# Kernel tuning notes

Measured on AMD Instinct MI355X. Metric: run time of the kernel, lower is better.

## Reference

```python
import jax, jax.numpy as jnp
import numpy as np

N = 50000
E = 800000
IN_C = 64
OUT_C = 64
K = 2
GATE_C = IN_C + OUT_C
LAMBDA_MAX = 2.0


def _lap_norm(edge_index, edge_weight, n):
    # PyG ChebConv norm: sym Laplacian L = I - D^-1/2 A D^-1/2, scaled 2L/lmax - I.
    # With lambda_max=2 the diagonal term is (2/lmax)*1 - 1 = 0, so only the
    # off-diagonal weights -(2/lmax) * w_norm remain.
    row, col = edge_index[0], edge_index[1]
    deg = jax.ops.segment_sum(edge_weight, row, num_segments=n)
    dinv = jnp.where(deg > 0, jax.lax.rsqrt(jnp.where(deg > 0, deg, 1.0)), 0.0)
    lw = -(2.0 / LAMBDA_MAX) * edge_weight * dinv[row] * dinv[col]
    diag = jnp.full((n,), 2.0 / LAMBDA_MAX - 1.0, edge_weight.dtype)  # zeros for lmax=2
    return row, col, lw, diag


def _cheb_conv(x, row, col, lw, diag, Ws, b):
    # Ws: [K, C_in, C_out]; Tx_0 = x, Tx_1 = L_hat x, Tx_k = 2 L_hat Tx_{k-1} - Tx_{k-2}
    n = x.shape[0]

    def prop(h):  # L_hat @ h  via edge gather/scatter + diagonal
        msg = lw[:, None] * h[col]                      # [E, C]
        return jax.ops.segment_sum(msg, row, num_segments=n) + diag[:, None] * h

    Tx0 = x
    out = Tx0 @ Ws[0]
    Tx1 = prop(x)
    out = out + Tx1 @ Ws[1]
    for k in range(2, K):
        Tx2 = 2.0 * prop(Tx1) - Tx0
        out = out + Tx2 @ Ws[k]
        Tx0, Tx1 = Tx1, Tx2
    return out + b


def setup_inputs() -> dict:
    key = jax.random.key(0)
    ks = jax.random.split(key, 10)
    scale = 1.0 / np.sqrt(GATE_C)
    x = jax.random.normal(ks[0], (N, IN_C), jnp.float32)
    edge_index = jax.random.randint(ks[1], (2, E), 0, N, jnp.int64)
    edge_weight = jax.random.uniform(ks[2], (E,), jnp.float32)
    hidden_state = jax.random.normal(ks[3], (N, OUT_C), jnp.float32)
    Wz = jax.random.normal(ks[4], (K, GATE_C, OUT_C), jnp.float32) * scale
    Wr = jax.random.normal(ks[5], (K, GATE_C, OUT_C), jnp.float32) * scale
    Wh = jax.random.normal(ks[6], (K, GATE_C, OUT_C), jnp.float32) * scale
    bz = jnp.zeros((OUT_C,), jnp.float32)
    br = jnp.zeros((OUT_C,), jnp.float32)
    bh = jnp.zeros((OUT_C,), jnp.float32)
    return {"x": x, "edge_index": edge_index, "edge_weight": edge_weight,
            "hidden_state": hidden_state, "Wz": Wz, "bz": bz,
            "Wr": Wr, "br": br, "Wh": Wh, "bh": bh}


def reference(x, edge_index, edge_weight, hidden_state, Wz, bz, Wr, br, Wh, bh):
    n = x.shape[0]
    row, col, lw, diag = _lap_norm(edge_index, edge_weight, n)
    gate_input = jnp.concatenate([x, hidden_state], axis=-1)          # [N, GATE_C]
    z = jax.nn.sigmoid(_cheb_conv(gate_input, row, col, lw, diag, Wz, bz))
    r = jax.nn.sigmoid(_cheb_conv(gate_input, row, col, lw, diag, Wr, br))
    cand_in = jnp.concatenate([x, r * hidden_state], axis=-1)
    h_tilde = jnp.tanh(_cheb_conv(cand_in, row, col, lw, diag, Wh, bh))
    return (1.0 - z) * hidden_state + z * h_tilde
```

## Files before the change

### kernel.cpp

```cpp
#include <hip/hip_runtime.h>
#include <cstdint>

#define N_NODES 50000
#define N_EDGES 800000
#define C 64
#define SLOTS 64
#define B_N 120
#define NB 417
#define PCAP 2560
#define STG_BLOCKS 126
#define STG_CHUNK 6350

typedef __attribute__((ext_vector_type(8))) short bf16x8;
typedef __attribute__((ext_vector_type(4))) float f32x4;

static constexpr size_t OFF_GCUR = 0;
static constexpr size_t OFF_DINV = 512;
static constexpr size_t OFF_CNT  = 50688;
static constexpr size_t OFF_BZR  = 100864;
static constexpr size_t OFF_BH   = 117248;
static constexpr size_t OFF_CSR  = 125440;
static constexpr size_t OFF_XH   = OFF_CSR + (size_t)N_NODES * 64;
static constexpr size_t OFF_XB   = OFF_XH + (size_t)N_NODES * C;
static constexpr size_t OFF_HB   = OFF_XB + (size_t)N_NODES * C / 2;
static constexpr size_t OFF_PXB  = OFF_HB + (size_t)N_NODES * C / 2;
static constexpr size_t OFF_PHB  = OFF_PXB + (size_t)N_NODES * C / 2;
static constexpr size_t OFF_RHB  = OFF_PHB + (size_t)N_NODES * C / 2;
static constexpr size_t OFF_RHD  = OFF_RHB + (size_t)N_NODES * C / 2;
static constexpr size_t OFF_STG  = OFF_PXB;

__device__ __forceinline__ short f2bf(float f) {
    unsigned u = __float_as_uint(f);
    u += 0x7fffu + ((u >> 16) & 1u);
    return (short)(u >> 16);
}
__device__ __forceinline__ float bf_lo(unsigned v) { return __uint_as_float(v << 16); }
__device__ __forceinline__ float bf_hi(unsigned v) { return __uint_as_float(v & 0xffff0000u); }
__device__ __forceinline__ float bfu(unsigned short v) { return __uint_as_float((unsigned)v << 16); }
__device__ __forceinline__ float fast_sigmoid(float v) { return 1.f / (1.f + __expf(-v)); }
__device__ __forceinline__ float fast_tanh(float v) { return 1.f - 2.f / (__expf(2.f * v) + 1.f); }

__global__ __launch_bounds__(256) void zero_pack_kernel(
        int* __restrict__ gcur,
        const float* __restrict__ Wz, const float* __restrict__ Wr,
        const float* __restrict__ Wh,
        short* __restrict__ Bzr, short* __restrict__ Bh) {
    if (blockIdx.x == 24) {
        gcur[threadIdx.x] = 0;
        gcur[256 + threadIdx.x] = 0;
        return;
    }
    int gid = blockIdx.x * 256 + threadIdx.x;
    if (gid < 4096) {
        int ktct = gid >> 6, lane = gid & 63;
        int kt = ktct >> 3, ct = ktct & 7;
        int colg = ct * 16 + (lane & 15);
        int k0 = kt * 32 + (lane >> 4) * 8;
        const float* W = (colg < 64) ? Wz : Wr;
        int c = colg & 63;
        short v[8];
        #pragma unroll
        for (int j = 0; j < 8; ++j) {
            int k = k0 + j;
            v[j] = f2bf(W[(k >> 7) * (128 * 64) + (k & 127) * 64 + c]);
        }
        *(bf16x8*)(Bzr + (size_t)ktct * 512 + lane * 8) = *(bf16x8*)v;
    } else {
        int idx = gid - 4096;
        int ktct = idx >> 6, lane = idx & 63;
        int kt = ktct >> 2, ct = ktct & 3;
        int colg = ct * 16 + (lane & 15);
        int k0 = kt * 32 + (lane >> 4) * 8;
        short v[8];
        #pragma unroll
        for (int j = 0; j < 8; ++j) {
            int k = k0 + j;
            v[j] = f2bf(Wh[(k >> 7) * (128 * 64) + (k & 127) * 64 + colg]);
        }
        *(bf16x8*)(Bh + (size_t)ktct * 512 + lane * 8) = *(bf16x8*)v;
    }
}

__global__ __launch_bounds__(512) void stage_kernel(
        const int* __restrict__ row, const int* __restrict__ col,
        const float* __restrict__ w,
        int* __restrict__ gcur, uint2* __restrict__ stg) {
    __shared__ int lcnt[NB];
    __shared__ int lbase[NB];
    int tid = threadIdx.x;
    int e0 = blockIdx.x * STG_CHUNK;
    int e1 = min(e0 + STG_CHUNK, N_EDGES);
    for (int i = tid; i < NB; i += 512) lcnt[i] = 0;
    __syncthreads();
    for (int e = e0 + tid; e < e1; e += 512)
        atomicAdd(&lcnt[row[e] / B_N], 1);
    __syncthreads();
    for (int i = tid; i < NB; i += 512) {
        int c = lcnt[i];
        lbase[i] = c ? atomicAdd(&gcur[i], c) : 0;
        lcnt[i] = 0;
    }
    __syncthreads();
    for (int e = e0 + tid; e < e1; e += 512) {
        int r = row[e];
        int b = r / B_N;
        int off = atomicAdd(&lcnt[b], 1);
        int pos = lbase[b] + off;
        unsigned cw = ((unsigned)col[e] << 16) | (unsigned short)f2bf(w[e]);
        if (pos < PCAP)
            stg[(size_t)b * PCAP + pos] = make_uint2((unsigned)(r - b * B_N), cw);
    }
}

__global__ __launch_bounds__(256) void sort_kernel(
        const int* __restrict__ gcur, const uint2* __restrict__ stg,
        const float* __restrict__ x, const float* __restrict__ h,
        unsigned* __restrict__ csr, int* __restrict__ cnt, float* __restrict__ dinv,
        unsigned* __restrict__ xh,
        unsigned short* __restrict__ xb, unsigned short* __restrict__ hb) {
    __shared__ int lcnt[B_N];
    __shared__ int lbase[B_N];
    __shared__ float ldeg[B_N];
    __shared__ float ldv[B_N];
    __shared__ int scanb[128];
    __shared__ unsigned lbuf[PCAP];
    __shared__ unsigned char lnode[PCAP];
    int b = blockIdx.x, tid = threadIdx.x;
    int n0 = b * B_N;
    int m = min(gcur[b], PCAP);
    for (int i = tid; i < B_N; i += 256) { lcnt[i] = 0; ldeg[i] = 0.f; }
    __syncthreads();
    const uint2* s = stg + (size_t)b * PCAP;
    for (int i = tid; i < m; i += 256) {
        uint2 e = s[i];
        atomicAdd(&lcnt[e.x], 1);
        atomicAdd(&ldeg[e.x], bf_lo(e.y));
    }
    __syncthreads();
    if (tid < 128) scanb[tid] = (tid < B_N) ? lcnt[tid] : 0;
    __syncthreads();
    for (int d = 1; d < 128; d <<= 1) {
        int v = 0;
        if (tid < 128 && tid >= d) v = scanb[tid - d];
        __syncthreads();
        if (tid < 128) scanb[tid] += v;
        __syncthreads();
    }
    if (tid < B_N) { lbase[tid] = scanb[tid] - lcnt[tid]; lcnt[tid] = 0; }
    __syncthreads();
    for (int i = tid; i < m; i += 256) {
        uint2 e = s[i];
        int off = atomicAdd(&lcnt[e.x], 1);
        int p = lbase[e.x] + off;
        lbuf[p] = e.y;
        lnode[p] = (unsigned char)e.x;
    }
    __syncthreads();
    for (int i = tid; i < m; i += 256) {
        int nl = lnode[i];
        int pos = i - lbase[nl];
        csr[(size_t)(n0 + nl) * SLOTS + pos] = lbuf[i];
    }
    if (tid < B_N) {
        int node = n0 + tid;
        if (node < N_NODES) {
            cnt[node] = lcnt[tid];
            float d = ldeg[tid];
            float dv = (d > 0.f) ? rsqrtf(d) : 0.f;
            dinv[node] = dv;
            ldv[tid] = dv;
        } else ldv[tid] = 0.f;
    }
    __syncthreads();
    for (int i = tid; i < B_N * 16; i += 256) {
        int g = n0 * 16 + i;
        if (g >= N_NODES * 16) continue;
        float dv = ldv[i >> 4];
        float4 xv = ((const float4*)x)[g];
        float4 hv = ((const float4*)h)[g];
        uint4 o;
        o.x = ((unsigned)(unsigned short)f2bf(hv.x * dv) << 16) | (unsigned short)f2bf(xv.x * dv);
        o.y = ((unsigned)(unsigned short)f2bf(hv.y * dv) << 16) | (unsigned short)f2bf(xv.y * dv);
        o.z = ((unsigned)(unsigned short)f2bf(hv.z * dv) << 16) | (unsigned short)f2bf(xv.z * dv);
        o.w = ((unsigned)(unsigned short)f2bf(hv.w * dv) << 16) | (unsigned short)f2bf(xv.w * dv);
        ((uint4*)xh)[g] = o;
        ((short4*)xb)[g] = make_short4(f2bf(xv.x), f2bf(xv.y), f2bf(xv.z), f2bf(xv.w));
        ((short4*)hb)[g] = make_short4(f2bf(hv.x), f2bf(hv.y), f2bf(hv.z), f2bf(hv.w));
    }
}

__global__ __launch_bounds__(256) void prop2_gather_kernel(
        const int* __restrict__ cnt, const unsigned* __restrict__ csr,
        const float* __restrict__ dinv, const unsigned* __restrict__ xh,
        unsigned short* __restrict__ Pxb, unsigned short* __restrict__ Phb) {
    int n = (blockIdx.x * 256 + threadIdx.x) >> 6;
    int lane = threadIdx.x & 63;
    if (n >= N_NODES) return;
    int m = min(cnt[n], SLOTS);
    const unsigned* s = csr + (size_t)n * SLOTS;
    float ax = 0.f, ah = 0.f;
    int e = 0;
    for (; e + 4 <= m; e += 4) {
        unsigned p0 = s[e], p1 = s[e + 1], p2 = s[e + 2], p3 = s[e + 3];
        unsigned v0 = xh[(p0 >> 16) * C + lane];
        unsigned v1 = xh[(p1 >> 16) * C + lane];
        unsigned v2 = xh[(p2 >> 16) * C + lane];
        unsigned v3 = xh[(p3 >> 16) * C + lane];
        float w0 = bf_lo(p0), w1 = bf_lo(p1), w2 = bf_lo(p2), w3 = bf_lo(p3);
        ax = fmaf(w0, bf_lo(v0), ax);  ah = fmaf(w0, bf_hi(v0), ah);
        ax = fmaf(w1, bf_lo(v1), ax);  ah = fmaf(w1, bf_hi(v1), ah);
        ax = fmaf(w2, bf_lo(v2), ax);  ah = fmaf(w2, bf_hi(v2), ah);
        ax = fmaf(w3, bf_lo(v3), ax);  ah = fmaf(w3, bf_hi(v3), ah);
    }
    for (; e < m; ++e) {
        unsigned p = s[e];
        unsigned v = xh[(p >> 16) * C + lane];
        float wv = bf_lo(p);
        ax = fmaf(wv, bf_lo(v), ax);
        ah = fmaf(wv, bf_hi(v), ah);
    }
    float sc = -dinv[n];
    Pxb[(size_t)n * C + lane] = (unsigned short)f2bf(sc * ax);
    Phb[(size_t)n * C + lane] = (unsigned short)f2bf(sc * ah);
}

__global__ __launch_bounds__(256) void prop1_gather_kernel(
        const int* __restrict__ cnt, const unsigned* __restrict__ csr,
        const float* __restrict__ dinv,
        const unsigned short* __restrict__ rhd, unsigned short* __restrict__ Prhb) {
    int n = (blockIdx.x * 256 + threadIdx.x) >> 6;
    int lane = threadIdx.x & 63;
    if (n >= N_NODES) return;
    int m = min(cnt[n], SLOTS);
    const unsigned* s = csr + (size_t)n * SLOTS;
    float acc = 0.f;
    int e = 0;
    for (; e + 4 <= m; e += 4) {
        unsigned p0 = s[e], p1 = s[e + 1], p2 = s[e + 2], p3 = s[e + 3];
        float v0 = bfu(rhd[(p0 >> 16) * C + lane]);
        float v1 = bfu(rhd[(p1 >> 16) * C + lane]);
        float v2 = bfu(rhd[(p2 >> 16) * C + lane]);
        float v3 = bfu(rhd[(p3 >> 16) * C + lane]);
        acc = fmaf(bf_lo(p0), v0, acc);
        acc = fmaf(bf_lo(p1), v1, acc);
        acc = fmaf(bf_lo(p2), v2, acc);
        acc = fmaf(bf_lo(p3), v3, acc);
    }
    for (; e < m; ++e) {
        unsigned p = s[e];
        acc = fmaf(bf_lo(p), bfu(rhd[(p >> 16) * C + lane]), acc);
    }
    Prhb[(size_t)n * C + lane] = (unsigned short)f2bf(-dinv[n] * acc);
}

__global__ __launch_bounds__(256) void gemm_zr_mfma_kernel(
        const unsigned short* __restrict__ xb, const unsigned short* __restrict__ hb,
        const unsigned short* __restrict__ Pxb, const unsigned short* __restrict__ Phb,
        const short* __restrict__ Bzr,
        const float* __restrict__ bz, const float* __restrict__ br,
        const float* __restrict__ dinv,
        float* __restrict__ z, unsigned short* __restrict__ rhb,
        unsigned short* __restrict__ rhd) {
    int wave = (blockIdx.x * 256 + threadIdx.x) >> 6;
    int lane = threadIdx.x & 63;
    int node0 = wave * 16;
    if (node0 >= N_NODES) return;
    int q = lane >> 4;
    int nodeA = node0 + (lane & 15);

    f32x4 acc[8];
    #pragma unroll
    for (int i = 0; i < 8; ++i) acc[i] = (f32x4){0.f, 0.f, 0.f, 0.f};

    const bf16x8* Bp = (const bf16x8*)Bzr;
    #pragma unroll
    for (int kt = 0; kt < 8; ++kt) {
        const unsigned short* src = (kt < 2) ? xb : (kt < 4) ? hb : (kt < 6) ? Pxb : Phb;
        bf16x8 a = *(const bf16x8*)(src + (size_t)nodeA * C + (kt & 1) * 32 + q * 8);
        #pragma unroll
        for (int ct = 0; ct < 8; ++ct) {
            bf16x8 bfr = Bp[(kt * 8 + ct) * 64 + lane];
            acc[ct] = __builtin_amdgcn_mfma_f32_16x16x32_bf16(a, bfr, acc[ct], 0, 0, 0);
        }
    }

    float dv[4];
    #pragma unroll
    for (int r = 0; r < 4; ++r) dv[r] = dinv[node0 + q * 4 + r];

    #pragma unroll
    for (int ct = 0; ct < 8; ++ct) {
        int colg = ct * 16 + (lane & 15);
        if (ct < 4) {
            float bias = bz[colg];
            #pragma unroll
            for (int r = 0; r < 4; ++r) {
                int node = node0 + q * 4 + r;
                z[(size_t)node * C + colg] = fast_sigmoid(acc[ct][r] + bias);
            }
        } else {
            int oc = colg - 64;
            float bias = br[oc];
            #pragma unroll
            for (int r = 0; r < 4; ++r) {
                int node = node0 + q * 4 + r;
                float sg = fast_sigmoid(acc[ct][r] + bias);
                float rhv = sg * bfu(hb[(size_t)node * C + oc]);
                rhb[(size_t)node * C + oc] = (unsigned short)f2bf(rhv);
                rhd[(size_t)node * C + oc] = (unsigned short)f2bf(rhv * dv[r]);
            }
        }
    }
}

__global__ __launch_bounds__(256) void gemm_h_mfma_kernel(
        const unsigned short* __restrict__ xb, const unsigned short* __restrict__ rhb,
        const unsigned short* __restrict__ Pxb, const unsigned short* __restrict__ Prhb,
        const short* __restrict__ Bh, const float* __restrict__ bh,
        const float* __restrict__ z,  const float* __restrict__ h,
        float* __restrict__ out) {
    int wave = (blockIdx.x * 256 + threadIdx.x) >> 6;
    int lane = threadIdx.x & 63;
    int node0 = wave * 16;
    if (node0 >= N_NODES) return;
    int q = lane >> 4;
    int nodeA = node0 + (lane & 15);

    f32x4 acc[4];
    #pragma unroll
    for (int i = 0; i < 4; ++i) acc[i] = (f32x4){0.f, 0.f, 0.f, 0.f};

    const bf16x8* Bp = (const bf16x8*)Bh;
    #pragma unroll
    for (int kt = 0; kt < 8; ++kt) {
        const unsigned short* src = (kt < 2) ? xb : (kt < 4) ? rhb : (kt < 6) ? Pxb : Prhb;
        bf16x8 a = *(const bf16x8*)(src + (size_t)nodeA * C + (kt & 1) * 32 + q * 8);
        #pragma unroll
        for (int ct = 0; ct < 4; ++ct) {
            bf16x8 bfr = Bp[(kt * 4 + ct) * 64 + lane];
            acc[ct] = __builtin_amdgcn_mfma_f32_16x16x32_bf16(a, bfr, acc[ct], 0, 0, 0);
        }
    }

    #pragma unroll
    for (int ct = 0; ct < 4; ++ct) {
        int oc = ct * 16 + (lane & 15);
        float bias = bh[oc];
        #pragma unroll
        for (int r = 0; r < 4; ++r) {
            int node = node0 + q * 4 + r;
            float ht = fast_tanh(acc[ct][r] + bias);
            float zz = z[(size_t)node * C + oc];
            float hv = h[(size_t)node * C + oc];
            out[(size_t)node * C + oc] = (1.f - zz) * hv + zz * ht;
        }
    }
}

extern "C" void kernel_launch(void* const* d_in, const int* in_sizes, int n_in,
                              void* d_out, int out_size, void* d_ws, size_t ws_size,
                              hipStream_t stream) {
    const float* x    = (const float*)d_in[0];
    const int*   eidx = (const int*)  d_in[1];
    const float* w    = (const float*)d_in[2];
    const float* h    = (const float*)d_in[3];
    const float* Wz   = (const float*)d_in[4];
    const float* bz   = (const float*)d_in[5];
    const float* Wr   = (const float*)d_in[6];
    const float* br   = (const float*)d_in[7];
    const float* Wh   = (const float*)d_in[8];
    const float* bh   = (const float*)d_in[9];
    float* out = (float*)d_out;
    float* ws  = (float*)d_ws;

    const int* row = eidx;
    const int* col = eidx + N_EDGES;

    int*            gcur = (int*)(ws + OFF_GCUR);
    float*          dinv = ws + OFF_DINV;
    int*            cnt  = (int*)(ws + OFF_CNT);
    unsigned*       csr  = (unsigned*)(ws + OFF_CSR);
    short*          Bzr  = (short*)(ws + OFF_BZR);
    short*          Bh   = (short*)(ws + OFF_BH);
    unsigned*       xh   = (unsigned*)(ws + OFF_XH);
    unsigned short* xb   = (unsigned short*)(ws + OFF_XB);
    unsigned short* hb   = (unsigned short*)(ws + OFF_HB);
    unsigned short* Pxb  = (unsigned short*)(ws + OFF_PXB);
    unsigned short* Phb  = (unsigned short*)(ws + OFF_PHB);
    unsigned short* rhb  = (unsigned short*)(ws + OFF_RHB);
    unsigned short* rhd  = (unsigned short*)(ws + OFF_RHD);
    uint2*          stg  = (uint2*)(ws + OFF_STG);
    float*          z    = out;

    zero_pack_kernel<<<25, 256, 0, stream>>>(gcur, Wz, Wr, Wh, Bzr, Bh);

    stage_kernel<<<STG_BLOCKS, 512, 0, stream>>>(row, col, w, gcur, stg);

    sort_kernel<<<NB, 256, 0, stream>>>(gcur, stg, x, h, csr, cnt, dinv, xh, xb, hb);

    prop2_gather_kernel<<<(N_NODES * 64 + 255) / 256, 256, 0, stream>>>(
        cnt, csr, dinv, xh, Pxb, Phb);

    {
        int waves = (N_NODES + 15) / 16;
        int blocks = (waves + 3) / 4;
        gemm_zr_mfma_kernel<<<blocks, 256, 0, stream>>>(
            xb, hb, Pxb, Phb, Bzr, bz, br, dinv, z, rhb, rhd);
    }

    prop1_gather_kernel<<<(N_NODES * 64 + 255) / 256, 256, 0, stream>>>(
        cnt, csr, dinv, rhd, Phb);

    {
        int waves = (N_NODES + 15) / 16;
        int blocks = (waves + 3) / 4;
        gemm_h_mfma_kernel<<<blocks, 256, 0, stream>>>(
            xb, rhb, Pxb, Phb, Bh, bh, z, h, out);
    }
}
```

Before: 230.6 us.

## Fuse neighbor gather propagation into the MFMA gate GEMM kernels via LDS

Removes the two standalone gather kernels and folds them into the z/r and candidate GEMM kernels. Each wave now gathers its 16 nodes' Laplacian-propagated features serially into shared memory, then feeds them straight to the MFMA loop. This drops the global write and re-read of the Phb/Prhb intermediates and two kernel launches. The price is far less parallelism in the latency-bound gather: roughly 3k waves instead of 50k, each walking 16 nodes in sequence. The inner loop is unrolled to 8 loads to partly make up for that.

After: 278.3 us. 1.21x slower.

```diff
diff --git a/kernel.cpp b/kernel.cpp
--- a/kernel.cpp
+++ b/kernel.cpp
@@ -10,6 +10,7 @@
 #define PCAP 2560
 #define STG_BLOCKS 126
 #define STG_CHUNK 6350
+#define LDW 72
 
 typedef __attribute__((ext_vector_type(8))) short bf16x8;
 typedef __attribute__((ext_vector_type(4))) float f32x4;
@@ -24,8 +25,7 @@
 static constexpr size_t OFF_XB   = OFF_XH + (size_t)N_NODES * C;
 static constexpr size_t OFF_HB   = OFF_XB + (size_t)N_NODES * C / 2;
 static constexpr size_t OFF_PXB  = OFF_HB + (size_t)N_NODES * C / 2;
-static constexpr size_t OFF_PHB  = OFF_PXB + (size_t)N_NODES * C / 2;
-static constexpr size_t OFF_RHB  = OFF_PHB + (size_t)N_NODES * C / 2;
+static constexpr size_t OFF_RHB  = OFF_PXB + (size_t)N_NODES * C / 2;
 static constexpr size_t OFF_RHD  = OFF_RHB + (size_t)N_NODES * C / 2;
 static constexpr size_t OFF_STG  = OFF_PXB;
 
@@ -189,94 +189,78 @@
     }
 }
 
-__global__ __launch_bounds__(256) void prop2_gather_kernel(
+__global__ __launch_bounds__(256) void gemm_zr_fused_kernel(
         const int* __restrict__ cnt, const unsigned* __restrict__ csr,
         const float* __restrict__ dinv, const unsigned* __restrict__ xh,
-        unsigned short* __restrict__ Pxb, unsigned short* __restrict__ Phb) {
-    int n = (blockIdx.x * 256 + threadIdx.x) >> 6;
-    int lane = threadIdx.x & 63;
-    if (n >= N_NODES) return;
-    int m = min(cnt[n], SLOTS);
-    const unsigned* s = csr + (size_t)n * SLOTS;
-    float ax = 0.f, ah = 0.f;
-    int e = 0;
-    for (; e + 4 <= m; e += 4) {
-        unsigned p0 = s[e], p1 = s[e + 1], p2 = s[e + 2], p3 = s[e + 3];
-        unsigned v0 = xh[(p0 >> 16) * C + lane];
-        unsigned v1 = xh[(p1 >> 16) * C + lane];
-        unsigned v2 = xh[(p2 >> 16) * C + lane];
-        unsigned v3 = xh[(p3 >> 16) * C + lane];
-        float w0 = bf_lo(p0), w1 = bf_lo(p1), w2 = bf_lo(p2), w3 = bf_lo(p3);
-        ax = fmaf(w0, bf_lo(v0), ax);  ah = fmaf(w0, bf_hi(v0), ah);
-        ax = fmaf(w1, bf_lo(v1), ax);  ah = fmaf(w1, bf_hi(v1), ah);
-        ax = fmaf(w2, bf_lo(v2), ax);  ah = fmaf(w2, bf_hi(v2), ah);
-        ax = fmaf(w3, bf_lo(v3), ax);  ah = fmaf(w3, bf_hi(v3), ah);
-    }
-    for (; e < m; ++e) {
-        unsigned p = s[e];
-        unsigned v = xh[(p >> 16) * C + lane];
-        float wv = bf_lo(p);
-        ax = fmaf(wv, bf_lo(v), ax);
-        ah = fmaf(wv, bf_hi(v), ah);
-    }
-    float sc = -dinv[n];
-    Pxb[(size_t)n * C + lane] = (unsigned short)f2bf(sc * ax);
-    Phb[(size_t)n * C + lane] = (unsigned short)f2bf(sc * ah);
-}
-
-__global__ __launch_bounds__(256) void prop1_gather_kernel(
-        const int* __restrict__ cnt, const unsigned* __restrict__ csr,
-        const float* __restrict__ dinv,
-        const unsigned short* __restrict__ rhd, unsigned short* __restrict__ Prhb) {
-    int n = (blockIdx.x * 256 + threadIdx.x) >> 6;
-    int lane = threadIdx.x & 63;
-    if (n >= N_NODES) return;
-    int m = min(cnt[n], SLOTS);
-    const unsigned* s = csr + (size_t)n * SLOTS;
-    float acc = 0.f;
-    int e = 0;
-    for (; e + 4 <= m; e += 4) {
-        unsigned p0 = s[e], p1 = s[e + 1], p2 = s[e + 2], p3 = s[e + 3];
-        float v0 = bfu(rhd[(p0 >> 16) * C + lane]);
-        float v1 = bfu(rhd[(p1 >> 16) * C + lane]);
-        float v2 = bfu(rhd[(p2 >> 16) * C + lane]);
-        float v3 = bfu(rhd[(p3 >> 16) * C + lane]);
-        acc = fmaf(bf_lo(p0), v0, acc);
-        acc = fmaf(bf_lo(p1), v1, acc);
-        acc = fmaf(bf_lo(p2), v2, acc);
-        acc = fmaf(bf_lo(p3), v3, acc);
-    }
-    for (; e < m; ++e) {
-        unsigned p = s[e];
-        acc = fmaf(bf_lo(p), bfu(rhd[(p >> 16) * C + lane]), acc);
-    }
-    Prhb[(size_t)n * C + lane] = (unsigned short)f2bf(-dinv[n] * acc);
-}
-
-__global__ __launch_bounds__(256) void gemm_zr_mfma_kernel(
         const unsigned short* __restrict__ xb, const unsigned short* __restrict__ hb,
-        const unsigned short* __restrict__ Pxb, const unsigned short* __restrict__ Phb,
         const short* __restrict__ Bzr,
         const float* __restrict__ bz, const float* __restrict__ br,
-        const float* __restrict__ dinv,
         float* __restrict__ z, unsigned short* __restrict__ rhb,
-        unsigned short* __restrict__ rhd) {
-    int wave = (blockIdx.x * 256 + threadIdx.x) >> 6;
-    int lane = threadIdx.x & 63;
+        unsigned short* __restrict__ rhd, unsigned short* __restrict__ Pxb) {
+    __shared__ unsigned short lPx[4][16][LDW];
+    __shared__ unsigned short lPh[4][16][LDW];
+    int tid = threadIdx.x;
+    int wv = tid >> 6, lane = tid & 63;
+    int wave = blockIdx.x * 4 + wv;
     int node0 = wave * 16;
     if (node0 >= N_NODES) return;
-    int q = lane >> 4;
-    int nodeA = node0 + (lane & 15);
-
+
+    for (int r = 0; r < 16; ++r) {
+        int node = node0 + r;
+        int m = min(cnt[node], SLOTS);
+        const unsigned* s = csr + (size_t)node * SLOTS;
+        float ax = 0.f, ah = 0.f;
+        int e = 0;
+        for (; e + 8 <= m; e += 8) {
+            unsigned p0 = s[e], p1 = s[e+1], p2 = s[e+2], p3 = s[e+3];
+            unsigned p4 = s[e+4], p5 = s[e+5], p6 = s[e+6], p7 = s[e+7];
+            unsigned v0 = xh[(p0 >> 16) * C + lane];
+            unsigned v1 = xh[(p1 >> 16) * C + lane];
+            unsigned v2 = xh[(p2 >> 16) * C + lane];
+            unsigned v3 = xh[(p3 >> 16) * C + lane];
+            unsigned v4 = xh[(p4 >> 16) * C + lane];
+            unsigned v5 = xh[(p5 >> 16) * C + lane];
+            unsigned v6 = xh[(p6 >> 16) * C + lane];
+            unsigned v7 = xh[(p7 >> 16) * C + lane];
+            ax = fmaf(bf_lo(p0), bf_lo(v0), ax);  ah = fmaf(bf_lo(p0), bf_hi(v0), ah);
+            ax = fmaf(bf_lo(p1), bf_lo(v1), ax);  ah = fmaf(bf_lo(p1), bf_hi(v1), ah);
+            ax = fmaf(bf_lo(p2), bf_lo(v2), ax);  ah = fmaf(bf_lo(p2), bf_hi(v2), ah);
+            ax = fmaf(bf_lo(p3), bf_lo(v3), ax);  ah = fmaf(bf_lo(p3), bf_hi(v3), ah);
+            ax = fmaf(bf_lo(p4), bf_lo(v4), ax);  ah = fmaf(bf_lo(p4), bf_hi(v4), ah);
+            ax = fmaf(bf_lo(p5), bf_lo(v5), ax);  ah = fmaf(bf_lo(p5), bf_hi(v5), ah);
+            ax = fmaf(bf_lo(p6), bf_lo(v6), ax);  ah = fmaf(bf_lo(p6), bf_hi(v6), ah);
+            ax = fmaf(bf_lo(p7), bf_lo(v7), ax);  ah = fmaf(bf_lo(p7), bf_hi(v7), ah);
+        }
+        for (; e < m; ++e) {
+            unsigned p = s[e];
+            unsigned v = xh[(p >> 16) * C + lane];
+            ax = fmaf(bf_lo(p), bf_lo(v), ax);
+            ah = fmaf(bf_lo(p), bf_hi(v), ah);
+        }
+        float sc = -dinv[node];
+        unsigned short pxv = (unsigned short)f2bf(sc * ax);
+        unsigned short phv = (unsigned short)f2bf(sc * ah);
+        lPx[wv][r][lane] = pxv;
+        lPh[wv][r][lane] = phv;
+        Pxb[(size_t)node * C + lane] = pxv;
+    }
+
+    int q = lane >> 4, am = lane & 15;
+    int nodeA = node0 + am;
     f32x4 acc[8];
     #pragma unroll
     for (int i = 0; i < 8; ++i) acc[i] = (f32x4){0.f, 0.f, 0.f, 0.f};
-
     const bf16x8* Bp = (const bf16x8*)Bzr;
     #pragma unroll
     for (int kt = 0; kt < 8; ++kt) {
-        const unsigned short* src = (kt < 2) ? xb : (kt < 4) ? hb : (kt < 6) ? Pxb : Phb;
-        bf16x8 a = *(const bf16x8*)(src + (size_t)nodeA * C + (kt & 1) * 32 + q * 8);
+        bf16x8 a;
+        if (kt < 4) {
+            const unsigned short* src = (kt < 2) ? xb : hb;
+            a = *(const bf16x8*)(src + (size_t)nodeA * C + (kt & 1) * 32 + q * 8);
+        } else {
+            const unsigned short* lsrc = (kt < 6) ? &lPx[wv][am][0] : &lPh[wv][am][0];
+            a = *(const bf16x8*)(lsrc + (kt & 1) * 32 + q * 8);
+        }
         #pragma unroll
         for (int ct = 0; ct < 8; ++ct) {
             bf16x8 bfr = Bp[(kt * 8 + ct) * 64 + lane];
@@ -313,28 +297,69 @@
     }
 }
 
-__global__ __launch_bounds__(256) void gemm_h_mfma_kernel(
+__global__ __launch_bounds__(256) void gemm_h_fused_kernel(
+        const int* __restrict__ cnt, const unsigned* __restrict__ csr,
+        const float* __restrict__ dinv, const unsigned short* __restrict__ rhd,
         const unsigned short* __restrict__ xb, const unsigned short* __restrict__ rhb,
-        const unsigned short* __restrict__ Pxb, const unsigned short* __restrict__ Prhb,
+        const unsigned short* __restrict__ Pxb,
         const short* __restrict__ Bh, const float* __restrict__ bh,
-        const float* __restrict__ z,  const float* __restrict__ h,
+        const float* __restrict__ z, const float* __restrict__ h,
         float* __restrict__ out) {
-    int wave = (blockIdx.x * 256 + threadIdx.x) >> 6;
-    int lane = threadIdx.x & 63;
+    __shared__ unsigned short lPr[4][16][LDW];
+    int tid = threadIdx.x;
+    int wv = tid >> 6, lane = tid & 63;
+    int wave = blockIdx.x * 4 + wv;
     int node0 = wave * 16;
     if (node0 >= N_NODES) return;
-    int q = lane >> 4;
-    int nodeA = node0 + (lane & 15);
-
+
+    for (int r = 0; r < 16; ++r) {
+        int node = node0 + r;
+        int m = min(cnt[node], SLOTS);
+        const unsigned* s = csr + (size_t)node * SLOTS;
+        float acc = 0.f;
+        int e = 0;
+        for (; e + 8 <= m; e += 8) {
+            unsigned p0 = s[e], p1 = s[e+1], p2 = s[e+2], p3 = s[e+3];
+            unsigned p4 = s[e+4], p5 = s[e+5], p6 = s[e+6], p7 = s[e+7];
+            float v0 = bfu(rhd[(p0 >> 16) * C + lane]);
+            float v1 = bfu(rhd[(p1 >> 16) * C + lane]);
+            float v2 = bfu(rhd[(p2 >> 16) * C + lane]);
+            float v3 = bfu(rhd[(p3 >> 16) * C + lane]);
+            float v4 = bfu(rhd[(p4 >> 16) * C + lane]);
+            float v5 = bfu(rhd[(p5 >> 16) * C + lane]);
+            float v6 = bfu(rhd[(p6 >> 16) * C + lane]);
+            float v7 = bfu(rhd[(p7 >> 16) * C + lane]);
+            acc = fmaf(bf_lo(p0), v0, acc);
+            acc = fmaf(bf_lo(p1), v1, acc);
+            acc = fmaf(bf_lo(p2), v2, acc);
+            acc = fmaf(bf_lo(p3), v3, acc);
+            acc = fmaf(bf_lo(p4), v4, acc);
+            acc = fmaf(bf_lo(p5), v5, acc);
+            acc = fmaf(bf_lo(p6), v6, acc);
+            acc = fmaf(bf_lo(p7), v7, acc);
+        }
+        for (; e < m; ++e) {
+            unsigned p = s[e];
+            acc = fmaf(bf_lo(p), bfu(rhd[(p >> 16) * C + lane]), acc);
+        }
+        lPr[wv][r][lane] = (unsigned short)f2bf(-dinv[node] * acc);
+    }
+
+    int q = lane >> 4, am = lane & 15;
+    int nodeA = node0 + am;
     f32x4 acc[4];
     #pragma unroll
     for (int i = 0; i < 4; ++i) acc[i] = (f32x4){0.f, 0.f, 0.f, 0.f};
-
     const bf16x8* Bp = (const bf16x8*)Bh;
     #pragma unroll
     for (int kt = 0; kt < 8; ++kt) {
-        const unsigned short* src = (kt < 2) ? xb : (kt < 4) ? rhb : (kt < 6) ? Pxb : Prhb;
-        bf16x8 a = *(const bf16x8*)(src + (size_t)nodeA * C + (kt & 1) * 32 + q * 8);
+        bf16x8 a;
+        if (kt < 6) {
+            const unsigned short* src = (kt < 2) ? xb : (kt < 4) ? rhb : Pxb;
+            a = *(const bf16x8*)(src + (size_t)nodeA * C + (kt & 1) * 32 + q * 8);
+        } else {
+            a = *(const bf16x8*)(&lPr[wv][am][0] + (kt & 1) * 32 + q * 8);
+        }
         #pragma unroll
         for (int ct = 0; ct < 4; ++ct) {
             bf16x8 bfr = Bp[(kt * 4 + ct) * 64 + lane];
@@ -386,7 +411,6 @@
     unsigned short* xb   = (unsigned short*)(ws + OFF_XB);
     unsigned short* hb   = (unsigned short*)(ws + OFF_HB);
     unsigned short* Pxb  = (unsigned short*)(ws + OFF_PXB);
-    unsigned short* Phb  = (unsigned short*)(ws + OFF_PHB);
     unsigned short* rhb  = (unsigned short*)(ws + OFF_RHB);
     unsigned short* rhd  = (unsigned short*)(ws + OFF_RHD);
     uint2*          stg  = (uint2*)(ws + OFF_STG);
@@ -398,23 +422,17 @@
 
     sort_kernel<<<NB, 256, 0, stream>>>(gcur, stg, x, h, csr, cnt, dinv, xh, xb, hb);
 
-    prop2_gather_kernel<<<(N_NODES * 64 + 255) / 256, 256, 0, stream>>>(
-        cnt, csr, dinv, xh, Pxb, Phb);
-
     {
         int waves = (N_NODES + 15) / 16;
         int blocks = (waves + 3) / 4;
-        gemm_zr_mfma_kernel<<<blocks, 256, 0, stream>>>(
-            xb, hb, Pxb, Phb, Bzr, bz, br, dinv, z, rhb, rhd);
-    }
-
-    prop1_gather_kernel<<<(N_NODES * 64 + 255) / 256, 256, 0, stream>>>(
-        cnt, csr, dinv, rhd, Phb);
+        gemm_zr_fused_kernel<<<blocks, 256, 0, stream>>>(
+            cnt, csr, dinv, xh, xb, hb, Bzr, bz, br, z, rhb, rhd, Pxb);
+    }
 
     {
         int waves = (N_NODES + 15) / 16;
         int blocks = (waves + 3) / 4;
-        gemm_h_mfma_kernel<<<blocks, 256, 0, stream>>>(
-            xb, rhb, Pxb, Phb, Bh, bh, z, h, out);
-    }
-}
+        gemm_h_fused_kernel<<<blocks, 256, 0, stream>>>(
+            cnt, csr, dinv, rhd, xb, rhb, Pxb, Bh, bh, z, h, out);
+    }
+}
```
